# Kernel tuning notes

Hardware: AMD Instinct MI355X
Metric: run time of the kernel (lower is better)

The kernel has to match this reference:

```python
import jax, jax.numpy as jnp
import numpy as np

D_MODEL = 1024
NUM_HEADS = 16
D_K = D_MODEL // NUM_HEADS


def setup_inputs() -> dict:
    key = jax.random.key(0)
    ks = jax.random.split(key, 9)
    B, S = 4, 2048
    scale = 1.0 / np.sqrt(D_MODEL)
    x = jax.random.normal(ks[0], (B, S, D_MODEL), dtype=jnp.float32)
    wq = jax.random.normal(ks[1], (D_MODEL, D_MODEL), dtype=jnp.float32) * scale
    wk = jax.random.normal(ks[2], (D_MODEL, D_MODEL), dtype=jnp.float32) * scale
    wv = jax.random.normal(ks[3], (D_MODEL, D_MODEL), dtype=jnp.float32) * scale
    wo = jax.random.normal(ks[4], (D_MODEL, D_MODEL), dtype=jnp.float32) * scale
    bq = jax.random.normal(ks[5], (D_MODEL,), dtype=jnp.float32) * 0.01
    bk = jax.random.normal(ks[6], (D_MODEL,), dtype=jnp.float32) * 0.01
    bv = jax.random.normal(ks[7], (D_MODEL,), dtype=jnp.float32) * 0.01
    bo = jax.random.normal(ks[8], (D_MODEL,), dtype=jnp.float32) * 0.01
    return {"x": x, "wq": wq, "bq": bq, "wk": wk, "bk": bk,
            "wv": wv, "bv": bv, "wo": wo, "bo": bo}


def reference(x, wq, bq, wk, bk, wv, bv, wo, bo):
    B, S, _ = x.shape
    # projections -> [B, H, S, d_k]
    def split_heads(t):
        return t.reshape(B, S, NUM_HEADS, D_K).transpose(0, 2, 1, 3)
    q = split_heads(x @ wq.T + bq)
    k = split_heads(x @ wk.T + bk)
    v = split_heads(x @ wv.T + bv)
    scores = jnp.einsum("bhqd,bhkd->bhqk", q, k) / np.sqrt(D_K).astype(np.float32)
    attn = jax.nn.softmax(scores, axis=-1)  # dropout is identity at eval
    out = jnp.einsum("bhqk,bhkd->bhqd", attn, v)
    out = out.transpose(0, 2, 1, 3).reshape(B, S, D_MODEL)
    return out @ wo.T + bo
```

## Files before the change

kernel.cpp:

```cpp
#include <hip/hip_runtime.h>

#define D_MODEL 1024
#define NHEADS  16
#define DK      64
#define BATCH   4
#define SEQ     2048
#define MROWS   (BATCH*SEQ)
#define BHCOUNT (BATCH*NHEADS)
#define KTILES  (SEQ/64)

typedef _Float16 half8 __attribute__((ext_vector_type(8)));
typedef _Float16 half4 __attribute__((ext_vector_type(4)));
typedef float    floatx4 __attribute__((ext_vector_type(4)));
typedef float    floatx16 __attribute__((ext_vector_type(16)));

__device__ __forceinline__ void load_lds16(const void* g, void* l) {
    __builtin_amdgcn_global_load_lds((const __attribute__((address_space(1))) void*)g,
                                     (__attribute__((address_space(3))) void*)l, 16, 0, 0);
}

__device__ __forceinline__ unsigned pkrtz_u32(float a, float b) {
    auto h = __builtin_amdgcn_cvt_pkrtz(a, b);
    union { decltype(h) v; unsigned u; } c; c.v = h; return c.u;
}

__device__ __forceinline__ int permrow(int r) {
    return (r & ~12) | ((r & 4) << 1) | ((r & 8) >> 1);
}

__global__ __launch_bounds__(256)
void cvt_f32_f16(const float* __restrict__ in, _Float16* __restrict__ out) {
    size_t i = ((size_t)blockIdx.x*256 + threadIdx.x)*4;
    float4 v = *(const float4*)(in + i);
    half4 h = {(_Float16)v.x, (_Float16)v.y, (_Float16)v.z, (_Float16)v.w};
    *(half4*)(out + i) = h;
}

__global__ __launch_bounds__(256)
void cvt4_f32_f16(const float* __restrict__ a, const float* __restrict__ b,
                  const float* __restrict__ c, const float* __restrict__ d,
                  _Float16* __restrict__ oa, _Float16* __restrict__ ob,
                  _Float16* __restrict__ oc, _Float16* __restrict__ od) {
    const float* src; _Float16* dst;
    switch (blockIdx.y) {
        case 0:  src=a; dst=oa; break;
        case 1:  src=b; dst=ob; break;
        case 2:  src=c; dst=oc; break;
        default: src=d; dst=od; break;
    }
    size_t i = ((size_t)blockIdx.x*256 + threadIdx.x)*4;
    float4 v = *(const float4*)(src + i);
    half4 h = {(_Float16)v.x, (_Float16)v.y, (_Float16)v.z, (_Float16)v.w};
    *(half4*)(dst + i) = h;
}

template<int MODE, int BK>
__global__ __launch_bounds__(256)
void gemm_nt_f16(const _Float16* __restrict__ A, const _Float16* __restrict__ W,
                 const float* __restrict__ b0, const float* __restrict__ b1,
                 const float* __restrict__ b2, void* __restrict__ Cout, float qscale)
{
    constexpr int GR  = BK/8;
    constexpr int NIT = BK/16;
    constexpr int NKT = 1024/BK;
    constexpr int KS  = BK/32;
    __shared__ _Float16 As[2][128*BK];
    __shared__ _Float16 Ws[2][128*BK];
    const int t = threadIdx.x;
    const int w = t >> 6, l = t & 63;
    const int wm = w >> 1, wn = w & 1;

    const int L   = blockIdx.x + (int)gridDim.x * blockIdx.y;
    const int nbx = gridDim.x;
    const int cpx = (int)(gridDim.x * gridDim.y) >> 3;
    const int wid = (L & 7) * cpx + (L >> 3);
    const int bn  = (wid % nbx) * 128;
    const int bm  = (wid / nbx) * 128;

    const int lrow = l & 15, lq4 = l >> 4;

    int srow[NIT], scol[NIT];
    #pragma unroll
    for (int it = 0; it < NIT; ++it) {
        int s = (it*4 + w)*64 + l;
        int r = s / GR, g = s % GR, gs;
        if constexpr (BK == 64) gs = g ^ (r & 7);
        else                    gs = g ^ ((r >> 1) & 3);
        srow[it] = r; scol[it] = gs*8;
    }

    floatx4 acc[4][4];
    #pragma unroll
    for (int i = 0; i < 4; ++i)
        #pragma unroll
        for (int j = 0; j < 4; ++j) acc[i][j] = (floatx4){0.f,0.f,0.f,0.f};

    #pragma unroll
    for (int it = 0; it < NIT; ++it) {
        load_lds16(A + (size_t)(bm + srow[it])*1024 + scol[it], &As[0][(it*4+w)*512]);
        load_lds16(W + (size_t)(bn + srow[it])*1024 + scol[it], &Ws[0][(it*4+w)*512]);
    }

    for (int kt = 0; kt < NKT; ++kt) {
        __syncthreads();
        const int cur = kt & 1;
        if (kt + 1 < NKT) {
            const int k1 = (kt + 1)*BK;
            #pragma unroll
            for (int it = 0; it < NIT; ++it) {
                load_lds16(A + (size_t)(bm + srow[it])*1024 + k1 + scol[it], &As[cur^1][(it*4+w)*512]);
                load_lds16(W + (size_t)(bn + srow[it])*1024 + k1 + scol[it], &Ws[cur^1][(it*4+w)*512]);
            }
        }
        #pragma unroll
        for (int ks = 0; ks < KS; ++ks) {
            int xg;
            if constexpr (BK == 64) xg = ((ks*4 + lq4) ^ (lrow & 7))*8;
            else                    xg = (lq4 ^ ((lrow >> 1) & 3))*8;
            half8 af[4], bf[4];
            #pragma unroll
            for (int i = 0; i < 4; ++i) af[i] = *(half8*)&As[cur][(wm*64 + i*16 + lrow)*BK + xg];
            #pragma unroll
            for (int j = 0; j < 4; ++j) bf[j] = *(half8*)&Ws[cur][(wn*64 + j*16 + lrow)*BK + xg];
            __builtin_amdgcn_s_setprio(1);
            #pragma unroll
            for (int i = 0; i < 4; ++i)
                #pragma unroll
                for (int j = 0; j < 4; ++j)
                    acc[i][j] = __builtin_amdgcn_mfma_f32_16x16x32_f16(af[i], bf[j], acc[i][j], 0, 0, 0);
            __builtin_amdgcn_s_setprio(0);
        }
    }

    constexpr size_t NXc = (size_t)MROWS * D_MODEL;
    const int which = bn >> 10;
    const float* bptr = (which == 0) ? b0 : (which == 1) ? b1 : b2;
    const float scale = (which == 0) ? qscale : 1.0f;
    #pragma unroll
    for (int j = 0; j < 4; ++j) {
        int gcol = bn + wn*64 + j*16 + lrow;
        float bv = bptr[gcol & 1023];
        #pragma unroll
        for (int i = 0; i < 4; ++i) {
            #pragma unroll
            for (int r = 0; r < 4; ++r) {
                int gm = bm + wm*64 + i*16 + lq4*4 + r;
                float val = (acc[i][j][r] + bv) * scale;
                if (MODE == 0) {
                    ((float*)Cout)[(size_t)gm*1024 + gcol] = val;
                } else {
                    int hc = gcol & 1023;
                    int b = gm >> 11, s = gm & 2047;
                    int h = hc >> 6, dk = hc & 63;
                    ((_Float16*)Cout)[which*NXc + (((size_t)(b*NHEADS + h))*SEQ + s)*DK + dk] = (_Float16)val;
                }
            }
        }
    }
}

__global__ __launch_bounds__(256)
void transpose_v(const _Float16* __restrict__ V, _Float16* __restrict__ Vt)
{
    __shared__ unsigned Lt[64][33];
    const int t = threadIdx.x;
    const int bh = blockIdx.y;
    const int s0 = blockIdx.x*64;
    const _Float16* Vb = V + ((size_t)bh*SEQ + s0)*DK;
    const int sp = t >> 3, dkc = (t & 7)*8;
    uint4 r0 = *(const uint4*)(Vb + (2*sp+0)*64 + dkc);
    uint4 r1 = *(const uint4*)(Vb + (2*sp+1)*64 + dkc);
    unsigned a0[4] = {r0.x, r0.y, r0.z, r0.w};
    unsigned a1[4] = {r1.x, r1.y, r1.z, r1.w};
    #pragma unroll
    for (int i = 0; i < 4; ++i) {
        Lt[dkc+2*i+0][sp] = (a0[i] & 0xFFFFu) | (a1[i] << 16);
        Lt[dkc+2*i+1][sp] = (a0[i] >> 16)     | (a1[i] & 0xFFFF0000u);
    }
    __syncthreads();
    const int dk = t >> 2, spc = (t & 3)*8;
    uint4 o0 = {Lt[dk][spc+0], Lt[dk][spc+1], Lt[dk][spc+2], Lt[dk][spc+3]};
    uint4 o1 = {Lt[dk][spc+4], Lt[dk][spc+5], Lt[dk][spc+6], Lt[dk][spc+7]};
    _Float16* dst = Vt + ((size_t)bh*DK + dk)*SEQ + s0 + spc*2;
    *(uint4*)(dst)     = o0;
    *(uint4*)(dst + 8) = o1;
}

__global__ __launch_bounds__(128)
void attn_mfma(const _Float16* __restrict__ Q, const _Float16* __restrict__ K,
               const _Float16* __restrict__ Vt, _Float16* __restrict__ AO)
{
    __shared__ _Float16 Ks[2][64*64];
    __shared__ _Float16 Vs[2][64*64];

    const int t = threadIdx.x;
    const int w = t >> 6, l = t & 63;
    const int l31 = l & 31, hi = l >> 5;

    const int L   = blockIdx.x + (int)gridDim.x * blockIdx.y;
    const int wid = (L & 7) * 128 + (L >> 3);
    const int bh  = wid >> 4;
    const int q0  = (wid & 15) * 128;

    const _Float16* Qb = Q  + ((size_t)bh*SEQ + q0)*DK;
    const _Float16* Kb = K  + (size_t)bh*SEQ*DK;
    const _Float16* Vb = Vt + (size_t)bh*DK*SEQ;

    int srow[4], scol[4], karow[4];
    #pragma unroll
    for (int it = 0; it < 4; ++it) {
        int s = (it*2 + w)*64 + l;
        int r = s >> 3;
        int lc = (s & 7) ^ (r & 7);
        srow[it] = r; scol[it] = lc*8;
        karow[it] = permrow(r);
    }

    half8 qf[2][4];
    #pragma unroll
    for (int qt = 0; qt < 2; ++qt)
        #pragma unroll
        for (int kk = 0; kk < 4; ++kk)
            qf[qt][kk] = *(const half8*)(Qb + (size_t)(w*64 + qt*32 + l31)*DK + kk*16 + hi*8);

    #pragma unroll
    for (int it = 0; it < 4; ++it) {
        load_lds16(Kb + (size_t)karow[it]*DK + scol[it], &Ks[0][(it*2+w)*512]);
        load_lds16(Vb + (size_t)srow[it]*SEQ + scol[it], &Vs[0][(it*2+w)*512]);
    }

    floatx16 Oacc[2][2];
    floatx16 lacc[2];
    #pragma unroll
    for (int qt = 0; qt < 2; ++qt) {
        #pragma unroll
        for (int i = 0; i < 16; ++i) { Oacc[qt][0][i] = 0.f; Oacc[qt][1][i] = 0.f; lacc[qt][i] = 0.f; }
    }
    floatx16 z16;
    #pragma unroll
    for (int i = 0; i < 16; ++i) z16[i] = 0.f;
    half8 onesf;
    #pragma unroll
    for (int i = 0; i < 8; ++i) onesf[i] = (_Float16)1.f;

#define ATTN_PREFETCH(NBUF, KT1)                                                          \
    if ((KT1) < KTILES) {                                                                 \
        _Pragma("unroll")                                                                 \
        for (int it = 0; it < 4; ++it) {                                                  \
            load_lds16(Kb + ((size_t)((KT1)*64 + karow[it]))*DK + scol[it],               \
                       &Ks[NBUF][(it*2+w)*512]);                                          \
            load_lds16(Vb + (size_t)srow[it]*SEQ + (KT1)*64 + scol[it],                   \
                       &Vs[NBUF][(it*2+w)*512]);                                          \
        }                                                                                 \
    }

#define ATTN_STEP(CUR, KT)                                                                \
    {                                                                                     \
        __syncthreads();                                                                  \
        ATTN_PREFETCH((CUR)^1, (KT)+1)                                                    \
        _Pragma("unroll")                                                                 \
        for (int kb = 0; kb < 2; ++kb) {                                                  \
            const int row = kb*32 + l31;                                                  \
                                \
            floatx16 sTa, sTb;                                                            \
            {                                                                             \
                half8 kf = *(half8*)&Ks[CUR][row*64 + ((hi ^ (row & 7)))*8];              \
                sTa = __builtin_amdgcn_mfma_f32_32x32x16_f16(kf, qf[0][0], z16, 0, 0, 0); \
                sTb = __builtin_amdgcn_mfma_f32_32x32x16_f16(kf, qf[1][0], z16, 0, 0, 0); \
            }                                                                             \
            _Pragma("unroll")                                                             \
            for (int kk = 1; kk < 4; ++kk) {                                              \
                half8 kf = *(half8*)&Ks[CUR][row*64 + (((kk*2 + hi) ^ (row & 7)))*8];     \
                sTa = __builtin_amdgcn_mfma_f32_32x32x16_f16(kf, qf[0][kk], sTa, 0, 0, 0);\
                sTb = __builtin_amdgcn_mfma_f32_32x32x16_f16(kf, qf[1][kk], sTb, 0, 0, 0);\
            }                                                                             \
                     \
            unsigned Wda[8], Wdb[8];                                                      \
            _Pragma("unroll")                                                             \
            for (int p = 0; p < 8; ++p) {                                                 \
                Wda[p] = pkrtz_u32(__builtin_amdgcn_exp2f(sTa[2*p]),                      \
                                   __builtin_amdgcn_exp2f(sTa[2*p+1]));                   \
                Wdb[p] = pkrtz_u32(__builtin_amdgcn_exp2f(sTb[2*p]),                      \
                                   __builtin_amdgcn_exp2f(sTb[2*p+1]));                   \
            }                                                                             \
                                     \
            _Pragma("unroll")                                                             \
            for (int kk2 = 0; kk2 < 2; ++kk2) {                                           \
                union { unsigned u[4]; half8 h; } pfa, pfb;                               \
                _Pragma("unroll")                                                         \
                for (int v = 0; v < 4; ++v) { pfa.u[v] = Wda[kk2*4 + v];                  \
                                              pfb.u[v] = Wdb[kk2*4 + v]; }                \
                lacc[0] = __builtin_amdgcn_mfma_f32_32x32x16_f16(pfa.h, onesf, lacc[0], 0, 0, 0); \
                lacc[1] = __builtin_amdgcn_mfma_f32_32x32x16_f16(pfb.h, onesf, lacc[1], 0, 0, 0); \
                const int vg = kb*4 + kk2*2 + hi;                                         \
                _Pragma("unroll")                                                         \
                for (int n = 0; n < 2; ++n) {                                             \
                    const int vrow = n*32 + l31;                                          \
                    half8 vf = *(half8*)&Vs[CUR][vrow*64 + ((vg ^ (vrow & 7)))*8];        \
                    Oacc[0][n] = __builtin_amdgcn_mfma_f32_32x32x16_f16(pfa.h, vf, Oacc[0][n], 0, 0, 0); \
                    Oacc[1][n] = __builtin_amdgcn_mfma_f32_32x32x16_f16(pfb.h, vf, Oacc[1][n], 0, 0, 0); \
                }                                                                         \
            }                                                                             \
        }                                                                                 \
    }

    for (int ktp = 0; ktp < KTILES; ktp += 2) {
        ATTN_STEP(0, ktp)
        ATTN_STEP(1, ktp+1)
    }
#undef ATTN_STEP
#undef ATTN_PREFETCH

    const int b = bh >> 4, h = bh & 15;
    #pragma unroll
    for (int qt = 0; qt < 2; ++qt)
        #pragma unroll
        for (int r = 0; r < 16; ++r) {
            float inv = 1.f / lacc[qt][r];
            int qrow = (r & 3) + 8*(r >> 2) + 4*hi;
            int gq = q0 + w*64 + qt*32 + qrow;
            _Float16* dst = AO + ((size_t)(b*SEQ + gq))*D_MODEL + h*DK;
            dst[l31]      = (_Float16)(Oacc[qt][0][r] * inv);
            dst[32 + l31] = (_Float16)(Oacc[qt][1][r] * inv);
        }
}

extern "C" void kernel_launch(void* const* d_in, const int* in_sizes, int n_in,
                              void* d_out, int out_size, void* d_ws, size_t ws_size,
                              hipStream_t stream)
{
    const float* x  = (const float*)d_in[0];
    const float* wq = (const float*)d_in[1];
    const float* bq = (const float*)d_in[2];
    const float* wk = (const float*)d_in[3];
    const float* bk = (const float*)d_in[4];
    const float* wv = (const float*)d_in[5];
    const float* bv = (const float*)d_in[6];
    const float* wo = (const float*)d_in[7];
    const float* bo = (const float*)d_in[8];

    const size_t NX = (size_t)MROWS * D_MODEL;
    const size_t NW = (size_t)D_MODEL * D_MODEL;
    _Float16* xh  = (_Float16*)d_ws;
    _Float16* wqh = xh  + NX;
    _Float16* wkh = wqh + NW;
    _Float16* wvh = wkh + NW;
    _Float16* woh = wvh + NW;
    _Float16* Qh  = woh + NW;
    _Float16* Kh  = Qh  + NX;
    _Float16* Vh  = Kh  + NX;
    _Float16* Vth = Vh  + NX;
    _Float16* AOh = Vth + NX;

    cvt_f32_f16<<<NX/1024, 256, 0, stream>>>(x, xh);
    cvt4_f32_f16<<<dim3(NW/1024, 4), 256, 0, stream>>>(wq, wk, wv, wo, wqh, wkh, wvh, woh);

    const float QSCALE = 0.125f * 1.44269504f;

    gemm_nt_f16<1,32><<<dim3(3*D_MODEL/128, MROWS/128), 256, 0, stream>>>(
        xh, wqh, bq, bk, bv, Qh, QSCALE);

    transpose_v<<<dim3(SEQ/64, BHCOUNT), 256, 0, stream>>>(Vh, Vth);
    attn_mfma<<<dim3(SEQ/128, BHCOUNT), 128, 0, stream>>>(Qh, Kh, Vth, AOh);

    gemm_nt_f16<0,64><<<dim3(D_MODEL/128, MROWS/128), 256, 0, stream>>>(
        AOh, woh, bo, bo, bo, d_out, 1.0f);
}
```

Before: 300.0 us.

## Widen attention blocks to four waves and compute softmax row sums with scalar adds

The attention kernel now runs 256-thread blocks covering 256 queries, so each K/V tile staged in LDS serves four waves instead of two. That halves global-to-LDS traffic per query and halves the number of blocks. The row-sum MFMAs against a ones vector are replaced by per-lane scalar accumulation of the exponentials. A cross-half shuffle and a per-row shuffle then apply the normalization at write-out. The change removes two MFMAs per sub-step, at the cost of extra VALU adds and a tighter register budget under launch_bounds(256,3).

```diff
diff --git a/kernel.cpp b/kernel.cpp
--- a/kernel.cpp
+++ b/kernel.cpp
@@ -186,7 +186,7 @@
     *(uint4*)(dst + 8) = o1;
 }
 
-__global__ __launch_bounds__(128)
+__global__ __launch_bounds__(256, 3)
 void attn_mfma(const _Float16* __restrict__ Q, const _Float16* __restrict__ K,
                const _Float16* __restrict__ Vt, _Float16* __restrict__ AO)
 {
@@ -198,18 +198,18 @@
     const int l31 = l & 31, hi = l >> 5;
 
     const int L   = blockIdx.x + (int)gridDim.x * blockIdx.y;
-    const int wid = (L & 7) * 128 + (L >> 3);
-    const int bh  = wid >> 4;
-    const int q0  = (wid & 15) * 128;
+    const int wid = (L & 7) * 64 + (L >> 3);
+    const int bh  = wid >> 3;
+    const int q0  = (wid & 7) * 256;
 
     const _Float16* Qb = Q  + ((size_t)bh*SEQ + q0)*DK;
     const _Float16* Kb = K  + (size_t)bh*SEQ*DK;
     const _Float16* Vb = Vt + (size_t)bh*DK*SEQ;
 
-    int srow[4], scol[4], karow[4];
-    #pragma unroll
-    for (int it = 0; it < 4; ++it) {
-        int s = (it*2 + w)*64 + l;
+    int srow[2], scol[2], karow[2];
+    #pragma unroll
+    for (int it = 0; it < 2; ++it) {
+        int s = (it*4 + w)*64 + l;
         int r = s >> 3;
         int lc = (s & 7) ^ (r & 7);
         srow[it] = r; scol[it] = lc*8;
@@ -224,33 +224,29 @@
             qf[qt][kk] = *(const half8*)(Qb + (size_t)(w*64 + qt*32 + l31)*DK + kk*16 + hi*8);
 
     #pragma unroll
-    for (int it = 0; it < 4; ++it) {
-        load_lds16(Kb + (size_t)karow[it]*DK + scol[it], &Ks[0][(it*2+w)*512]);
-        load_lds16(Vb + (size_t)srow[it]*SEQ + scol[it], &Vs[0][(it*2+w)*512]);
+    for (int it = 0; it < 2; ++it) {
+        load_lds16(Kb + (size_t)karow[it]*DK + scol[it], &Ks[0][(it*4+w)*512]);
+        load_lds16(Vb + (size_t)srow[it]*SEQ + scol[it], &Vs[0][(it*4+w)*512]);
     }
 
     floatx16 Oacc[2][2];
-    floatx16 lacc[2];
-    #pragma unroll
-    for (int qt = 0; qt < 2; ++qt) {
-        #pragma unroll
-        for (int i = 0; i < 16; ++i) { Oacc[qt][0][i] = 0.f; Oacc[qt][1][i] = 0.f; lacc[qt][i] = 0.f; }
-    }
+    #pragma unroll
+    for (int qt = 0; qt < 2; ++qt)
+        #pragma unroll
+        for (int i = 0; i < 16; ++i) { Oacc[qt][0][i] = 0.f; Oacc[qt][1][i] = 0.f; }
+    float psum[2] = {0.f, 0.f};
     floatx16 z16;
     #pragma unroll
     for (int i = 0; i < 16; ++i) z16[i] = 0.f;
-    half8 onesf;
-    #pragma unroll
-    for (int i = 0; i < 8; ++i) onesf[i] = (_Float16)1.f;
 
 #define ATTN_PREFETCH(NBUF, KT1)                                                          \
     if ((KT1) < KTILES) {                                                                 \
         _Pragma("unroll")                                                                 \
-        for (int it = 0; it < 4; ++it) {                                                  \
+        for (int it = 0; it < 2; ++it) {                                                  \
             load_lds16(Kb + ((size_t)((KT1)*64 + karow[it]))*DK + scol[it],               \
-                       &Ks[NBUF][(it*2+w)*512]);                                          \
+                       &Ks[NBUF][(it*4+w)*512]);                                          \
             load_lds16(Vb + (size_t)srow[it]*SEQ + (KT1)*64 + scol[it],                   \
-                       &Vs[NBUF][(it*2+w)*512]);                                          \
+                       &Vs[NBUF][(it*4+w)*512]);                                          \
         }                                                                                 \
     }
 
@@ -278,20 +274,22 @@
             unsigned Wda[8], Wdb[8];                                                      \
             _Pragma("unroll")                                                             \
             for (int p = 0; p < 8; ++p) {                                                 \
-                Wda[p] = pkrtz_u32(__builtin_amdgcn_exp2f(sTa[2*p]),                      \
-                                   __builtin_amdgcn_exp2f(sTa[2*p+1]));                   \
-                Wdb[p] = pkrtz_u32(__builtin_amdgcn_exp2f(sTb[2*p]),                      \
-                                   __builtin_amdgcn_exp2f(sTb[2*p+1]));                   \
+                float a0 = __builtin_amdgcn_exp2f(sTa[2*p]);                              \
+                float a1 = __builtin_amdgcn_exp2f(sTa[2*p+1]);                            \
+                psum[0] += a0 + a1;                                                       \
+                Wda[p] = pkrtz_u32(a0, a1);                                               \
+                float b0 = __builtin_amdgcn_exp2f(sTb[2*p]);                              \
+                float b1 = __builtin_amdgcn_exp2f(sTb[2*p+1]);                            \
+                psum[1] += b0 + b1;                                                       \
+                Wdb[p] = pkrtz_u32(b0, b1);                                               \
             }                                                                             \
-                                     \
+                                                   \
             _Pragma("unroll")                                                             \
             for (int kk2 = 0; kk2 < 2; ++kk2) {                                           \
                 union { unsigned u[4]; half8 h; } pfa, pfb;                               \
                 _Pragma("unroll")                                                         \
                 for (int v = 0; v < 4; ++v) { pfa.u[v] = Wda[kk2*4 + v];                  \
                                               pfb.u[v] = Wdb[kk2*4 + v]; }                \
-                lacc[0] = __builtin_amdgcn_mfma_f32_32x32x16_f16(pfa.h, onesf, lacc[0], 0, 0, 0); \
-                lacc[1] = __builtin_amdgcn_mfma_f32_32x32x16_f16(pfb.h, onesf, lacc[1], 0, 0, 0); \
                 const int vg = kb*4 + kk2*2 + hi;                                         \
                 _Pragma("unroll")                                                         \
                 for (int n = 0; n < 2; ++n) {                                             \
@@ -313,16 +311,19 @@
 
     const int b = bh >> 4, h = bh & 15;
     #pragma unroll
-    for (int qt = 0; qt < 2; ++qt)
+    for (int qt = 0; qt < 2; ++qt) {
+        float lsum = psum[qt] + __shfl_xor(psum[qt], 32, 64);
+        float inv = 1.f / lsum;
         #pragma unroll
         for (int r = 0; r < 16; ++r) {
-            float inv = 1.f / lacc[qt][r];
             int qrow = (r & 3) + 8*(r >> 2) + 4*hi;
+            float invr = __shfl(inv, qrow, 64);
             int gq = q0 + w*64 + qt*32 + qrow;
             _Float16* dst = AO + ((size_t)(b*SEQ + gq))*D_MODEL + h*DK;
-            dst[l31]      = (_Float16)(Oacc[qt][0][r] * inv);
-            dst[32 + l31] = (_Float16)(Oacc[qt][1][r] * inv);
+            dst[l31]      = (_Float16)(Oacc[qt][0][r] * invr);
+            dst[32 + l31] = (_Float16)(Oacc[qt][1][r] * invr);
         }
+    }
 }
 
 extern "C" void kernel_launch(void* const* d_in, const int* in_sizes, int n_in,
@@ -361,7 +362,7 @@
         xh, wqh, bq, bk, bv, Qh, QSCALE);
 
     transpose_v<<<dim3(SEQ/64, BHCOUNT), 256, 0, stream>>>(Vh, Vth);
-    attn_mfma<<<dim3(SEQ/128, BHCOUNT), 128, 0, stream>>>(Qh, Kh, Vth, AOh);
+    attn_mfma<<<dim3(SEQ/256, BHCOUNT), 256, 0, stream>>>(Qh, Kh, Vth, AOh);
 
     gemm_nt_f16<0,64><<<dim3(D_MODEL/128, MROWS/128), 256, 0, stream>>>(
         AOh, woh, bo, bo, bo, d_out, 1.0f);
```

Result: slower. 366.8 us (+22.3%).
